# Kernel optimization log

Hardware: AMD Instinct MI355X
Metric: run time of the kernel (lower is better)

The kernel has to match this reference:

```python
import jax, jax.numpy as jnp
import numpy as np

B, S, H, W = 16, 512, 768, 8


def _enumerate_spans(S, W):
    # same enumeration order as the torch triple loop: for i, for j in [i, min(i+W, S)-1]
    starts, widths = [], []
    for i in range(S):
        for w in range(1, min(W, S - i) + 1):
            starts.append(i)
            widths.append(w)
    return np.asarray(starts, np.int32), np.asarray(widths, np.int32)


def setup_inputs() -> dict:
    key = jax.random.key(0)
    k1, k2, k3 = jax.random.split(key, 3)
    embeddings = jax.random.normal(k1, (B, S, H), dtype=jnp.float32)
    w_lin = jax.random.normal(k2, (2 * H + 1, H), dtype=jnp.float32) * 0.02
    b_lin = jax.random.normal(k3, (H,), dtype=jnp.float32) * 0.02
    starts, widths = _enumerate_spans(S, W)
    return {
        "embeddings": embeddings,
        "w_lin": w_lin,
        "b_lin": b_lin,
        "span_starts": jnp.asarray(starts),
        "span_widths": jnp.asarray(widths),
    }


def reference(embeddings, w_lin, b_lin, span_starts, span_widths):
    Bb, Ss, Hh = embeddings.shape
    cls_emb = embeddings[:, 0, :]  # [B, H]

    # Sliding-window running max: pooled[k, b, i, :] = max(embeddings[b, i:i+k+1, :])
    neg = jnp.full((Bb, W - 1, Hh), -jnp.inf, embeddings.dtype)
    padded = jnp.concatenate([embeddings, neg], axis=1)  # [B, S+W-1, H]
    cm = embeddings
    pools = [cm]
    for k in range(1, W):
        cm = jnp.maximum(cm, padded[:, k:k + Ss, :])
        pools.append(cm)
    pooled = jnp.stack(pools, axis=0)  # [W, B, S, H]

    # Gather each span's max-pooled embedding: [N, B, H] -> [B, N, H]
    span_max = pooled[span_widths - 1, :, span_starts, :]
    span_max = jnp.transpose(span_max, (1, 0, 2))

    N = span_starts.shape[0]
    cls_b = jnp.broadcast_to(cls_emb[:, None, :], (Bb, N, Hh))
    width_f = jnp.broadcast_to(
        span_widths.astype(embeddings.dtype)[None, :, None], (Bb, N, 1))
    feats = jnp.concatenate([span_max, cls_b, width_f], axis=-1)  # [B, N, 2H+1]

    span_reps = jnp.einsum("bnf,fh->bnh", feats, w_lin) + b_lin
    token_inputs = cls_emb  # [B, H]
    return token_inputs, span_reps.reshape(Bb * N, Hh)
```

## Files before the change

### kernel.cpp

```cpp
#include <hip/hip_runtime.h>
#include <hip/hip_bf16.h>
#include <stdint.h>

#define AS1 __attribute__((address_space(1)))
#define AS3 __attribute__((address_space(3)))

typedef float  f32x4  __attribute__((ext_vector_type(4)));
typedef __bf16 bf16x8 __attribute__((ext_vector_type(8)));
typedef __bf16 bf16x4 __attribute__((ext_vector_type(4)));
typedef short  s16x8  __attribute__((ext_vector_type(8)));

static constexpr int Bc = 16, Sc = 512, Hc = 768, NSPAN = 4068;
static constexpr int BM = 128, BN = 128, BK = 64, KS = Hc / BK;

__global__ __launch_bounds__(256)
void prep_w1t(const float* __restrict__ w_lin, unsigned short* __restrict__ w1t) {
  __shared__ __align__(16) unsigned short T[64][80];
  int bidk = blockIdx.x % 12, bidn = blockIdx.x / 12;
  int k0 = bidk * 64, n0 = bidn * 64;
  int tid = threadIdx.x;
#pragma unroll
  for (int p = 0; p < 16; ++p) {
    int idx = p * 256 + tid;
    int kl = idx >> 6, nl = idx & 63;
    float v = w_lin[(size_t)(k0 + kl) * Hc + (n0 + nl)];
    __bf16 bv = (__bf16)v;
    T[nl][kl] = __builtin_bit_cast(unsigned short, bv);
  }
  __syncthreads();
#pragma unroll
  for (int qq = 0; qq < 2; ++qq) {
    int q = qq * 256 + tid;
    int nl = q >> 3, c = q & 7;
    int n = n0 + nl;
    int gp = (k0 >> 3) + (c ^ (n & 7));
    s16x8 v = *(const s16x8*)(&T[nl][c * 8]);
    *(s16x8*)(w1t + (size_t)n * Hc + gp * 8) = v;
  }
}

__global__ __launch_bounds__(256)
void cls_proj_kernel(const float* __restrict__ emb, const float* __restrict__ w_lin,
                     const float* __restrict__ b_lin, float* __restrict__ out,
                     float* __restrict__ cls_proj) {
  __shared__ float cls_s[Hc];
  int b = blockIdx.x / 3, hc = blockIdx.x % 3;
  int tid = threadIdx.x;
  const float* cls = emb + (size_t)b * Sc * Hc;
  for (int i = tid; i < Hc; i += 256) cls_s[i] = cls[i];
  __syncthreads();
  int h = hc * 256 + tid;
  const float* wp = w_lin + (size_t)Hc * Hc + h;
  float p0 = 0, p1 = 0, p2 = 0, p3 = 0, p4 = 0, p5 = 0, p6 = 0, p7 = 0;
  for (int f = 0; f < Hc; f += 8) {
    p0 += cls_s[f + 0] * wp[(size_t)(f + 0) * Hc];
    p1 += cls_s[f + 1] * wp[(size_t)(f + 1) * Hc];
    p2 += cls_s[f + 2] * wp[(size_t)(f + 2) * Hc];
    p3 += cls_s[f + 3] * wp[(size_t)(f + 3) * Hc];
    p4 += cls_s[f + 4] * wp[(size_t)(f + 4) * Hc];
    p5 += cls_s[f + 5] * wp[(size_t)(f + 5) * Hc];
    p6 += cls_s[f + 6] * wp[(size_t)(f + 6) * Hc];
    p7 += cls_s[f + 7] * wp[(size_t)(f + 7) * Hc];
  }
  float acc = b_lin[h] + (((p0 + p1) + (p2 + p3)) + ((p4 + p5) + (p6 + p7)));
  cls_proj[b * Hc + h] = acc;
  out[b * Hc + h] = cls_s[h];
}

__global__ __launch_bounds__(256, 3)
void span_gemm(const float* __restrict__ emb, const unsigned short* __restrict__ w1t,
               const float* __restrict__ cls_proj, const float* __restrict__ w_lin,
               float* __restrict__ out) {
  __shared__ __align__(16) unsigned short Ald[BM * BK];
  __shared__ __align__(16) unsigned short Bld[BN * BK];

  int wg = blockIdx.x;
  int wgid = (wg & 7) * 384 + (wg >> 3);
  int tile_n = wgid % 6, tile_m = wgid / 6;
  int b = tile_m >> 5;
  int s0 = (tile_m & 31) << 4;
  int n0 = tile_n << 7;
  int tid = threadIdx.x;
  int wid = tid >> 6, lane = tid & 63;
  int wave_m = wid >> 1, wave_n = wid & 1;
  int lq = lane >> 4, lr = lane & 15;

  const char* embC = (const char*)(emb + (size_t)b * Sc * Hc);

  int bi = tid >> 4, bkq = tid & 15;
  uint32_t rowoff[8];
#pragma unroll
  for (int t = 0; t < 8; ++t) {
    int r = s0 + bi + t;
    if (r > 511) r = 511;
    rowoff[t] = (uint32_t)r * (Hc * 4) + bkq * 16;
  }
  int awbase = (bi << 10) + ((bkq & 1) << 3);

  f32x4 acc[4][4];
  f32x4 zer = {0.f, 0.f, 0.f, 0.f};
#pragma unroll
  for (int i = 0; i < 4; ++i)
#pragma unroll
    for (int j = 0; j < 4; ++j) acc[i][j] = zer;

  for (int ks = 0; ks < KS; ++ks) {
    int k0 = ks * BK;

    f32x4 rv[8];
#pragma unroll
    for (int t = 0; t < 8; ++t)
      rv[t] = *(const f32x4*)(embC + rowoff[t] + k0 * 4);

    __syncthreads();

#pragma unroll
    for (int j = 0; j < 4; ++j) {
      int u = (wid << 2) + j;
      int n = n0 + (u << 3) + (lane >> 3);
      const unsigned short* gp = w1t + (size_t)n * Hc + k0 + ((lane & 7) << 3);
      __builtin_amdgcn_global_load_lds((const AS1 uint32_t*)gp,
                                       (AS3 uint32_t*)(Bld + (u << 9)), 16, 0, 0);
    }

    {
      f32x4 cm = rv[0];
#pragma unroll
      for (int t = 0; t < 8; ++t) {
        if (t) {
          cm[0] = fmaxf(cm[0], rv[t][0]);
          cm[1] = fmaxf(cm[1], rv[t][1]);
          cm[2] = fmaxf(cm[2], rv[t][2]);
          cm[3] = fmaxf(cm[3], rv[t][3]);
        }
        bf16x4 p;
        p[0] = (__bf16)cm[0]; p[1] = (__bf16)cm[1];
        p[2] = (__bf16)cm[2]; p[3] = (__bf16)cm[3];
        int off = awbase + (t << 7) + ((((bkq >> 1) ^ t)) << 4);
        *(uint2*)((char*)Ald + off) = __builtin_bit_cast(uint2, p);
      }
    }

    __syncthreads();

#pragma unroll
    for (int kk = 0; kk < 2; ++kk) {
      bf16x8 af[4], bfr[4];
      int cf = (kk << 2) + lq;
#pragma unroll
      for (int mi = 0; mi < 4; ++mi) {
        int m = (wave_m << 6) + (mi << 4) + lr;
        af[mi] = *(const bf16x8*)((const char*)Ald + (m << 7) + ((cf ^ (m & 7)) << 4));
      }
#pragma unroll
      for (int ni = 0; ni < 4; ++ni) {
        int n = (wave_n << 6) + (ni << 4) + lr;
        bfr[ni] = *(const bf16x8*)((const char*)Bld + (n << 7) + ((cf ^ (n & 7)) << 4));
      }
#pragma unroll
      for (int mi = 0; mi < 4; ++mi)
#pragma unroll
        for (int ni = 0; ni < 4; ++ni)
          acc[mi][ni] = __builtin_amdgcn_mfma_f32_16x16x32_bf16(af[mi], bfr[ni], acc[mi][ni], 0, 0, 0);
    }
  }

  const float* w2p = w_lin + (size_t)(2 * Hc) * Hc;
  float* outp = out + Bc * Hc;
  int swb = (tile_m & 31) << 7;
#pragma unroll
  for (int ni = 0; ni < 4; ++ni) {
    int h = n0 + (wave_n << 6) + (ni << 4) + lr;
    float cp = cls_proj[b * Hc + h];
    float w2 = w2p[h];
#pragma unroll
    for (int mi = 0; mi < 4; ++mi) {
#pragma unroll
      for (int j = 0; j < 4; ++j) {
        int m = (wave_m << 6) + (mi << 4) + (lq << 2) + j;
        int sw = swb + m;
        int s = sw >> 3, w = (sw & 7) + 1;
        if (s + w <= 512) {
          int nsp = (s <= 504) ? (sw)
                               : (NSPAN - (((512 - s) * (513 - s)) >> 1) + w - 1);
          size_t oidx = ((size_t)b * NSPAN + nsp) * Hc + h;
          outp[oidx] = acc[mi][ni][j] + cp + (float)w * w2;
        }
      }
    }
  }
}

extern "C" void kernel_launch(void* const* d_in, const int* in_sizes, int n_in,
                              void* d_out, int out_size, void* d_ws, size_t ws_size,
                              hipStream_t stream) {
  const float* emb = (const float*)d_in[0];
  const float* w_lin = (const float*)d_in[1];
  const float* b_lin = (const float*)d_in[2];
  unsigned short* w1t = (unsigned short*)d_ws;
  float* cls_proj = (float*)((char*)d_ws + (size_t)Hc * Hc * 2);
  float* out = (float*)d_out;

  hipLaunchKernelGGL(prep_w1t, dim3(144), dim3(256), 0, stream, w_lin, w1t);
  hipLaunchKernelGGL(cls_proj_kernel, dim3(48), dim3(256), 0, stream, emb, w_lin, b_lin, out, cls_proj);
  hipLaunchKernelGGL(span_gemm, dim3(512 * 6), dim3(256), 0, stream, emb, w1t, cls_proj, w_lin, out);
}
```

Measured before the change: 152.5 us.

## Make span GEMM waves independent with per-wave LDS and direct B register loads

Restructures the span GEMM so each wave owns 8 sequence rows (64 span rows) with its own LDS A tile, and loads W1^T fragments straight from global memory into registers. All __syncthreads are removed. The workgroup tile grows to 256x128 with BK=32, which halves the grid. The trade-off is more register pressure (32 accumulators per wave, occupancy hint lowered to 2) and uncoalesced global B loads that are no longer shared through LDS across waves.

After: 213.2 us. +39.8%, slower.

```diff
diff --git a/kernel.cpp b/kernel.cpp
--- a/kernel.cpp
+++ b/kernel.cpp
@@ -1,9 +1,6 @@
 #include <hip/hip_runtime.h>
 #include <hip/hip_bf16.h>
 #include <stdint.h>
-
-#define AS1 __attribute__((address_space(1)))
-#define AS3 __attribute__((address_space(3)))
 
 typedef float  f32x4  __attribute__((ext_vector_type(4)));
 typedef __bf16 bf16x8 __attribute__((ext_vector_type(8)));
@@ -11,7 +8,7 @@
 typedef short  s16x8  __attribute__((ext_vector_type(8)));
 
 static constexpr int Bc = 16, Sc = 512, Hc = 768, NSPAN = 4068;
-static constexpr int BM = 128, BN = 128, BK = 64, KS = Hc / BK;
+static constexpr int BK = 32, KS = Hc / BK;
 
 __global__ __launch_bounds__(256)
 void prep_w1t(const float* __restrict__ w_lin, unsigned short* __restrict__ w1t) {
@@ -33,9 +30,8 @@
     int q = qq * 256 + tid;
     int nl = q >> 3, c = q & 7;
     int n = n0 + nl;
-    int gp = (k0 >> 3) + (c ^ (n & 7));
     s16x8 v = *(const s16x8*)(&T[nl][c * 8]);
-    *(s16x8*)(w1t + (size_t)n * Hc + gp * 8) = v;
+    *(s16x8*)(w1t + (size_t)n * Hc + k0 + c * 8) = v;
   }
 }
 
@@ -67,61 +63,58 @@
   out[b * Hc + h] = cls_s[h];
 }
 
-__global__ __launch_bounds__(256, 3)
+__global__ __launch_bounds__(256, 2)
 void span_gemm(const float* __restrict__ emb, const unsigned short* __restrict__ w1t,
                const float* __restrict__ cls_proj, const float* __restrict__ w_lin,
                float* __restrict__ out) {
-  __shared__ __align__(16) unsigned short Ald[BM * BK];
-  __shared__ __align__(16) unsigned short Bld[BN * BK];
+  __shared__ __align__(16) unsigned short Ald[4][2048];
 
   int wg = blockIdx.x;
-  int wgid = (wg & 7) * 384 + (wg >> 3);
-  int tile_n = wgid % 6, tile_m = wgid / 6;
-  int b = tile_m >> 5;
-  int s0 = (tile_m & 31) << 4;
-  int n0 = tile_n << 7;
+  int wgid = (wg & 7) * 192 + (wg >> 3);
+  int n_t = wgid % 6, mt_blk = wgid / 6;
+  int b = mt_blk >> 4;
   int tid = threadIdx.x;
   int wid = tid >> 6, lane = tid & 63;
-  int wave_m = wid >> 1, wave_n = wid & 1;
   int lq = lane >> 4, lr = lane & 15;
+  int n0 = n_t << 7;
+  int s_loc0 = ((mt_blk & 15) << 5) + (wid << 3);
 
   const char* embC = (const char*)(emb + (size_t)b * Sc * Hc);
+  char* Aw = (char*)Ald[wid];
 
-  int bi = tid >> 4, bkq = tid & 15;
+  int bi = lane >> 3, kq = lane & 7;
   uint32_t rowoff[8];
 #pragma unroll
   for (int t = 0; t < 8; ++t) {
-    int r = s0 + bi + t;
+    int r = s_loc0 + bi + t;
     if (r > 511) r = 511;
-    rowoff[t] = (uint32_t)r * (Hc * 4) + bkq * 16;
+    rowoff[t] = (uint32_t)r * (Hc * 4) + kq * 16;
   }
-  int awbase = (bi << 10) + ((bkq & 1) << 3);
+  int awbase = (bi << 9) + ((kq & 1) << 3);
 
-  f32x4 acc[4][4];
+  const unsigned short* bb = w1t + (size_t)(n0 + lr) * Hc + (lq << 3);
+
+  f32x4 acc[4][8];
   f32x4 zer = {0.f, 0.f, 0.f, 0.f};
 #pragma unroll
   for (int i = 0; i < 4; ++i)
 #pragma unroll
-    for (int j = 0; j < 4; ++j) acc[i][j] = zer;
+    for (int j = 0; j < 8; ++j) acc[i][j] = zer;
 
-  for (int ks = 0; ks < KS; ++ks) {
-    int k0 = ks * BK;
+  int arbase = (lr << 6) + (((lq ^ (lr & 3))) << 4);
+
+  for (int kt = 0; kt < KS; ++kt) {
+    int kb = kt << 7;
 
     f32x4 rv[8];
 #pragma unroll
     for (int t = 0; t < 8; ++t)
-      rv[t] = *(const f32x4*)(embC + rowoff[t] + k0 * 4);
+      rv[t] = *(const f32x4*)(embC + rowoff[t] + kb);
 
-    __syncthreads();
-
+    bf16x8 bfr[8];
 #pragma unroll
-    for (int j = 0; j < 4; ++j) {
-      int u = (wid << 2) + j;
-      int n = n0 + (u << 3) + (lane >> 3);
-      const unsigned short* gp = w1t + (size_t)n * Hc + k0 + ((lane & 7) << 3);
-      __builtin_amdgcn_global_load_lds((const AS1 uint32_t*)gp,
-                                       (AS3 uint32_t*)(Bld + (u << 9)), 16, 0, 0);
-    }
+    for (int ni = 0; ni < 8; ++ni)
+      bfr[ni] = *(const bf16x8*)(const void*)(bb + ni * 16 * Hc + kt * 32);
 
     {
       f32x4 cm = rv[0];
@@ -136,56 +129,48 @@
         bf16x4 p;
         p[0] = (__bf16)cm[0]; p[1] = (__bf16)cm[1];
         p[2] = (__bf16)cm[2]; p[3] = (__bf16)cm[3];
-        int off = awbase + (t << 7) + ((((bkq >> 1) ^ t)) << 4);
-        *(uint2*)((char*)Ald + off) = __builtin_bit_cast(uint2, p);
+        int off = awbase + (t << 6) + ((((kq >> 1) ^ t) & 3) << 4);
+        *(uint2*)(Aw + off) = __builtin_bit_cast(uint2, p);
       }
     }
 
-    __syncthreads();
-
+    bf16x8 af[4];
 #pragma unroll
-    for (int kk = 0; kk < 2; ++kk) {
-      bf16x8 af[4], bfr[4];
-      int cf = (kk << 2) + lq;
+    for (int mi = 0; mi < 4; ++mi)
+      af[mi] = *(const bf16x8*)(Aw + (mi << 10) + arbase);
 #pragma unroll
-      for (int mi = 0; mi < 4; ++mi) {
-        int m = (wave_m << 6) + (mi << 4) + lr;
-        af[mi] = *(const bf16x8*)((const char*)Ald + (m << 7) + ((cf ^ (m & 7)) << 4));
-      }
+    for (int mi = 0; mi < 4; ++mi)
 #pragma unroll
-      for (int ni = 0; ni < 4; ++ni) {
-        int n = (wave_n << 6) + (ni << 4) + lr;
-        bfr[ni] = *(const bf16x8*)((const char*)Bld + (n << 7) + ((cf ^ (n & 7)) << 4));
-      }
-#pragma unroll
-      for (int mi = 0; mi < 4; ++mi)
-#pragma unroll
-        for (int ni = 0; ni < 4; ++ni)
-          acc[mi][ni] = __builtin_amdgcn_mfma_f32_16x16x32_bf16(af[mi], bfr[ni], acc[mi][ni], 0, 0, 0);
-    }
+      for (int ni = 0; ni < 8; ++ni)
+        acc[mi][ni] = __builtin_amdgcn_mfma_f32_16x16x32_bf16(af[mi], bfr[ni], acc[mi][ni], 0, 0, 0);
   }
 
   const float* w2p = w_lin + (size_t)(2 * Hc) * Hc;
   float* outp = out + Bc * Hc;
-  int swb = (tile_m & 31) << 7;
+  int swb = s_loc0 << 3;
+  float cp[8], w2[8];
 #pragma unroll
-  for (int ni = 0; ni < 4; ++ni) {
-    int h = n0 + (wave_n << 6) + (ni << 4) + lr;
-    float cp = cls_proj[b * Hc + h];
-    float w2 = w2p[h];
+  for (int ni = 0; ni < 8; ++ni) {
+    int h = n0 + (ni << 4) + lr;
+    cp[ni] = cls_proj[b * Hc + h];
+    w2[ni] = w2p[h];
+  }
+  int hbase = n0 + lr;
 #pragma unroll
-    for (int mi = 0; mi < 4; ++mi) {
+  for (int mi = 0; mi < 4; ++mi) {
 #pragma unroll
-      for (int j = 0; j < 4; ++j) {
-        int m = (wave_m << 6) + (mi << 4) + (lq << 2) + j;
-        int sw = swb + m;
-        int s = sw >> 3, w = (sw & 7) + 1;
-        if (s + w <= 512) {
-          int nsp = (s <= 504) ? (sw)
-                               : (NSPAN - (((512 - s) * (513 - s)) >> 1) + w - 1);
-          size_t oidx = ((size_t)b * NSPAN + nsp) * Hc + h;
-          outp[oidx] = acc[mi][ni][j] + cp + (float)w * w2;
-        }
+    for (int j = 0; j < 4; ++j) {
+      int m = (mi << 4) + (lq << 2) + j;
+      int sw = swb + m;
+      int s = sw >> 3, w = (sw & 7) + 1;
+      if (s + w <= 512) {
+        int nsp = (s <= 504) ? sw
+                             : (NSPAN - (((512 - s) * (513 - s)) >> 1) + w - 1);
+        float* rowp = outp + ((size_t)b * NSPAN + nsp) * Hc + hbase;
+        float wf = (float)w;
+#pragma unroll
+        for (int ni = 0; ni < 8; ++ni)
+          rowp[ni << 4] = acc[mi][ni][j] + cp[ni] + wf * w2[ni];
       }
     }
   }
@@ -203,5 +188,5 @@
 
   hipLaunchKernelGGL(prep_w1t, dim3(144), dim3(256), 0, stream, w_lin, w1t);
   hipLaunchKernelGGL(cls_proj_kernel, dim3(48), dim3(256), 0, stream, emb, w_lin, b_lin, out, cls_proj);
-  hipLaunchKernelGGL(span_gemm, dim3(512 * 6), dim3(256), 0, stream, emb, w1t, cls_proj, w_lin, out);
+  hipLaunchKernelGGL(span_gemm, dim3(1536), dim3(256), 0, stream, emb, w1t, cls_proj, w_lin, out);
 }
```
